# Kernel tuning notes

Measured on AMD Instinct MI355X. Metric: run time of the kernel, lower is better.

Reference implementation:

```python
import jax, jax.numpy as jnp
import numpy as np

D_MODEL = 1024
N_HEADS = 16
D_K = D_MODEL // N_HEADS
B, S = 4, 2048


def setup_inputs() -> dict:
    key = jax.random.key(0)
    ks = jax.random.split(key, 5)
    scale = 1.0 / np.sqrt(D_MODEL)  # ~xavier scale for square matrices
    return {
        "Q": jax.random.normal(ks[0], (B, S, D_MODEL), dtype=jnp.float32),
        "length": jax.random.randint(ks[1], (B,), 1, S, dtype=jnp.int32),
        "Wq": jax.random.normal(ks[2], (D_MODEL, D_MODEL), dtype=jnp.float32) * scale,
        "bq": jnp.zeros((D_MODEL,), dtype=jnp.float32),
        "Wk": jax.random.normal(ks[3], (D_MODEL, D_MODEL), dtype=jnp.float32) * scale,
        "bk": jnp.zeros((D_MODEL,), dtype=jnp.float32),
        "Wv": jax.random.normal(ks[4], (D_MODEL, D_MODEL), dtype=jnp.float32) * scale,
        "bv": jnp.zeros((D_MODEL,), dtype=jnp.float32),
    }


def reference(Q, length, Wq, bq, Wk, bk, Wv, bv):
    b, s, d = Q.shape
    q_a = Q @ Wq + bq                                   # [b, s, d]
    # split heads: [b, h, s, d_k]
    q_s = q_a.reshape(b, s, N_HEADS, D_K).transpose(0, 2, 1, 3)
    k_s = (Q @ Wk + bk).reshape(b, s, N_HEADS, D_K).transpose(0, 2, 1, 3)
    v_s = (Q @ Wv + bv).reshape(b, s, N_HEADS, D_K).transpose(0, 2, 1, 3)

    # unnormalized exp attention with multiplicative key mask (faithful to source)
    scores = jnp.einsum("bhqd,bhkd->bhqk", q_s, k_s) / np.sqrt(D_K)
    scores = jnp.exp(scores)
    key_mask = (jnp.arange(s)[None, :] < length[:, None]).astype(scores.dtype)  # [b, k]
    scores = scores * key_mask[:, None, None, :]        # broadcast over heads, queries
    attn = scores / (jnp.sum(scores, axis=-1, keepdims=True) + 1e-8)
    context = jnp.einsum("bhqk,bhkd->bhqd", attn, v_s)
    context = context.transpose(0, 2, 1, 3).reshape(b, s, d)
    return context, q_a
```

## Files before the change

### kernel.cpp

```cpp
#include <hip/hip_runtime.h>

#define D_MODEL 1024
#define N_HEADS 16
#define D_KH    64
#define BATCH   4
#define SEQ     2048
#define M_TOTAL (BATCH*SEQ)

typedef __attribute__((ext_vector_type(8))) short short8;
typedef __attribute__((ext_vector_type(4))) float f32x4;
typedef __attribute__((ext_vector_type(4))) unsigned short u16x4;

__device__ __forceinline__ unsigned short f2bf(float f) {
  union { float f; unsigned u; } v; v.f = f;
  unsigned r = v.u + 0x7FFFu + ((v.u >> 16) & 1u);
  return (unsigned short)(r >> 16);
}

__global__ __launch_bounds__(256) void cvt_q(const float* __restrict__ Q,
                                             unsigned short* __restrict__ Qbf) {
  size_t i = (size_t)blockIdx.x * 256 + threadIdx.x;
  float4 v = ((const float4*)Q)[i];
  u16x4 o;
  o[0] = f2bf(v.x); o[1] = f2bf(v.y); o[2] = f2bf(v.z); o[3] = f2bf(v.w);
  ((u16x4*)Qbf)[i] = o;
}

__global__ __launch_bounds__(256) void cvt_wt(const float* __restrict__ Wq,
                                              const float* __restrict__ Wk,
                                              const float* __restrict__ Wv,
                                              unsigned short* __restrict__ WT) {
  const int z = blockIdx.z;
  const float* W = (z == 0) ? Wq : (z == 1) ? Wk : Wv;
  __shared__ float tile[32][33];
  const int k0 = blockIdx.y * 32, n0 = blockIdx.x * 32;
  const int tx = threadIdx.x & 31, ty = threadIdx.x >> 5;
  for (int i = 0; i < 4; ++i)
    tile[ty + i * 8][tx] = W[(size_t)(k0 + ty + i * 8) * D_MODEL + n0 + tx];
  __syncthreads();
  unsigned short* out = WT + (size_t)z * D_MODEL * D_MODEL;
  for (int i = 0; i < 4; ++i)
    out[(size_t)(n0 + ty + i * 8) * D_MODEL + k0 + tx] = f2bf(tile[tx][ty + i * 8]);
}

#define BM 128
#define BN 128
#define BK 32

__global__ __launch_bounds__(256, 2) void gemm_qkv(
    const unsigned short* __restrict__ Qbf,
    const unsigned short* __restrict__ WT,
    const float* __restrict__ bq_p, const float* __restrict__ bk_p,
    const float* __restrict__ bv_p,
    float* __restrict__ out_qa,
    unsigned short* __restrict__ kbf,
    unsigned short* __restrict__ vt) {
  const int z  = blockIdx.z;
  const int n0 = blockIdx.x * BN;
  const int m0 = blockIdx.y * BM;
  const int K  = D_MODEL;

  __shared__ unsigned short smA[BM * BK];
  __shared__ unsigned short smB[BN * BK];

  const int t    = threadIdx.x;
  const int lane = t & 63;
  const int w    = t >> 6;
  const int quad = lane >> 4;
  const int l16  = lane & 15;
  const int wr   = w >> 1, wc = w & 1;

  const unsigned short* Wz = WT + (size_t)z * D_MODEL * D_MODEL;

  f32x4 acc[4][4];
  for (int i = 0; i < 4; ++i)
    for (int j = 0; j < 4; ++j) acc[i][j] = (f32x4){0.f, 0.f, 0.f, 0.f};

  for (int k0 = 0; k0 < K; k0 += BK) {
    __syncthreads();
    for (int it = 0; it < 2; ++it) {
      int c   = t + it * 256;
      int row = c >> 2, col = (c & 3) * 8;
      const unsigned short* ga = Qbf + (size_t)(m0 + row) * K + k0 + col;
      const unsigned short* gb = Wz  + (size_t)(n0 + row) * K + k0 + col;
      __builtin_amdgcn_global_load_lds(
          (const __attribute__((address_space(1))) void*)ga,
          (__attribute__((address_space(3))) void*)&smA[c * 8], 16, 0, 0);
      __builtin_amdgcn_global_load_lds(
          (const __attribute__((address_space(1))) void*)gb,
          (__attribute__((address_space(3))) void*)&smB[c * 8], 16, 0, 0);
    }
    __syncthreads();

    short8 afr[4], bfr[4];
    for (int mi = 0; mi < 4; ++mi)
      afr[mi] = *(const short8*)&smA[(wr * 64 + mi * 16 + l16) * BK + quad * 8];
    for (int ni = 0; ni < 4; ++ni)
      bfr[ni] = *(const short8*)&smB[(wc * 64 + ni * 16 + l16) * BK + quad * 8];
    for (int mi = 0; mi < 4; ++mi)
      for (int ni = 0; ni < 4; ++ni)
        acc[mi][ni] = __builtin_amdgcn_mfma_f32_16x16x32_bf16(
            afr[mi], bfr[ni], acc[mi][ni], 0, 0, 0);
  }

  const float* bias = (z == 0) ? bq_p : (z == 1) ? bk_p : bv_p;
  if (z == 2) {
    for (int ni = 0; ni < 4; ++ni) {
      int n = n0 + wc * 64 + ni * 16 + l16;
      float bval = bias[n];
      int h = n >> 6, d = n & 63;
      for (int mi = 0; mi < 4; ++mi) {
        int m = m0 + wr * 64 + mi * 16 + quad * 4;
        int b = m >> 11, s = m & 2047;
        u16x4 o;
        for (int j = 0; j < 4; ++j) o[j] = f2bf(acc[mi][ni][j] + bval);
        *(u16x4*)&vt[(size_t)((b * 16 + h) * 64 + d) * SEQ + s] = o;
      }
    }
  } else {
    for (int ni = 0; ni < 4; ++ni) {
      int n = n0 + wc * 64 + ni * 16 + l16;
      float bval = bias[n];
      for (int mi = 0; mi < 4; ++mi) {
        int mbase = m0 + wr * 64 + mi * 16 + quad * 4;
        for (int j = 0; j < 4; ++j) {
          float v = acc[mi][ni][j] + bval;
          size_t idx = (size_t)(mbase + j) * D_MODEL + n;
          if (z == 0) out_qa[idx] = v;
          else        kbf[idx] = f2bf(v);
        }
      }
    }
  }
}

#define PSTR 72

__global__ __launch_bounds__(256, 2) void attn(
    const float* __restrict__ qa,
    const unsigned short* __restrict__ kbf,
    const unsigned short* __restrict__ vt,
    const int* __restrict__ length,
    float* __restrict__ ctx) {
  const int qt = blockIdx.x;
  const int bh = blockIdx.y;
  const int b = bh >> 4, h = bh & 15;
  const int len = length[b];

  const int t    = threadIdx.x;
  const int lane = t & 63;
  const int w    = t >> 6;
  const int quad = lane >> 4;
  const int l16  = lane & 15;

  __shared__ unsigned short sQ[64 * 64];
  __shared__ unsigned short sK[64 * 64];
  __shared__ unsigned short sVT[64 * 64];
  __shared__ unsigned short sP[64 * PSTR];

  {
    int r = t >> 2, c0 = (t & 3) * 16;
    const float* src = qa + (size_t)(b * SEQ + qt * 64 + r) * D_MODEL + h * D_KH + c0;
    unsigned short* dst = &sQ[r * 64 + c0];
    for (int i = 0; i < 4; ++i) {
      float4 v = *(const float4*)(src + i * 4);
      dst[i * 4 + 0] = f2bf(v.x); dst[i * 4 + 1] = f2bf(v.y);
      dst[i * 4 + 2] = f2bf(v.z); dst[i * 4 + 3] = f2bf(v.w);
    }
  }

  f32x4 accpv[4];
  for (int i = 0; i < 4; ++i) accpv[i] = (f32x4){0.f, 0.f, 0.f, 0.f};
  float den[4] = {0.f, 0.f, 0.f, 0.f};

  const float SCL = 0.125f * 1.44269504f;

  const int nkt = (len + 63) >> 6;
  for (int kt = 0; kt < nkt; ++kt) {
    __syncthreads();
    {
      int r = t >> 2, c0 = (t & 3) * 16;
      size_t koff = (size_t)(b * SEQ + kt * 64 + r) * D_MODEL + h * D_KH + c0;
      *(short8*)&sK[r * 64 + c0]     = *(const short8*)(kbf + koff);
      *(short8*)&sK[r * 64 + c0 + 8] = *(const short8*)(kbf + koff + 8);
      size_t voff = (size_t)(bh * 64 + r) * SEQ + kt * 64 + c0;
      *(short8*)&sVT[r * 64 + c0]     = *(const short8*)(vt + voff);
      *(short8*)&sVT[r * 64 + c0 + 8] = *(const short8*)(vt + voff + 8);
    }
    __syncthreads();

    short8 qa0 = *(const short8*)&sQ[(w * 16 + l16) * 64 + quad * 8];
    short8 qa1 = *(const short8*)&sQ[(w * 16 + l16) * 64 + 32 + quad * 8];
    for (int n = 0; n < 4; ++n) {
      f32x4 s = (f32x4){0.f, 0.f, 0.f, 0.f};
      short8 kb0 = *(const short8*)&sK[(n * 16 + l16) * 64 + quad * 8];
      short8 kb1 = *(const short8*)&sK[(n * 16 + l16) * 64 + 32 + quad * 8];
      s = __builtin_amdgcn_mfma_f32_16x16x32_bf16(qa0, kb0, s, 0, 0, 0);
      s = __builtin_amdgcn_mfma_f32_16x16x32_bf16(qa1, kb1, s, 0, 0, 0);
      int key = kt * 64 + n * 16 + l16;
      bool valid = key < len;
      for (int j = 0; j < 4; ++j) {
        float e = valid ? exp2f(s[j] * SCL) : 0.f;
        den[j] += e;
        sP[(w * 16 + quad * 4 + j) * PSTR + n * 16 + l16] = f2bf(e);
      }
    }

    short8 pa0 = *(const short8*)&sP[(w * 16 + l16) * PSTR + quad * 8];
    short8 pa1 = *(const short8*)&sP[(w * 16 + l16) * PSTR + 32 + quad * 8];
    for (int n2 = 0; n2 < 4; ++n2) {
      short8 vb0 = *(const short8*)&sVT[(n2 * 16 + l16) * 64 + quad * 8];
      short8 vb1 = *(const short8*)&sVT[(n2 * 16 + l16) * 64 + 32 + quad * 8];
      accpv[n2] = __builtin_amdgcn_mfma_f32_16x16x32_bf16(pa0, vb0, accpv[n2], 0, 0, 0);
      accpv[n2] = __builtin_amdgcn_mfma_f32_16x16x32_bf16(pa1, vb1, accpv[n2], 0, 0, 0);
    }
  }

  float inv[4];
  for (int j = 0; j < 4; ++j) {
    float d = den[j];
    d += __shfl_xor(d, 1, 64);
    d += __shfl_xor(d, 2, 64);
    d += __shfl_xor(d, 4, 64);
    d += __shfl_xor(d, 8, 64);
    inv[j] = 1.f / (d + 1e-8f);
  }
  for (int n2 = 0; n2 < 4; ++n2)
    for (int j = 0; j < 4; ++j) {
      int q = qt * 64 + w * 16 + quad * 4 + j;
      int d = h * D_KH + n2 * 16 + l16;
      ctx[(size_t)(b * SEQ + q) * D_MODEL + d] = accpv[n2][j] * inv[j];
    }
}

extern "C" void kernel_launch(void* const* d_in, const int* in_sizes, int n_in,
                              void* d_out, int out_size, void* d_ws, size_t ws_size,
                              hipStream_t stream) {
  const float* Q      = (const float*)d_in[0];
  const int*   length = (const int*)d_in[1];
  const float* Wq     = (const float*)d_in[2];
  const float* bq     = (const float*)d_in[3];
  const float* Wk     = (const float*)d_in[4];
  const float* bk     = (const float*)d_in[5];
  const float* Wv     = (const float*)d_in[6];
  const float* bv     = (const float*)d_in[7];

  float* out_ctx = (float*)d_out;
  float* out_qa  = out_ctx + (size_t)M_TOTAL * D_MODEL;

  char* ws = (char*)d_ws;
  unsigned short* Qbf = (unsigned short*)ws;
  unsigned short* WT  = (unsigned short*)(ws + (size_t)16 * 1024 * 1024);
  unsigned short* Kbf = (unsigned short*)(ws + (size_t)22 * 1024 * 1024);
  unsigned short* Vt  = (unsigned short*)(ws + (size_t)38 * 1024 * 1024);

  hipLaunchKernelGGL(cvt_q, dim3((M_TOTAL * D_MODEL) / (256 * 4)), dim3(256), 0, stream,
                     Q, Qbf);
  hipLaunchKernelGGL(cvt_wt, dim3(32, 32, 3), dim3(256), 0, stream, Wq, Wk, Wv, WT);
  hipLaunchKernelGGL(gemm_qkv, dim3(D_MODEL / BN, M_TOTAL / BM, 3), dim3(256), 0, stream,
                     Qbf, WT, bq, bk, bv, out_qa, Kbf, Vt);
  hipLaunchKernelGGL(attn, dim3(SEQ / 64, BATCH * N_HEADS), dim3(256), 0, stream,
                     out_qa, Kbf, Vt, length, out_ctx);
}
```

Before: 300.2 us.

## Transpose attention MFMAs, pad LDS tiles, pack P stores and vectorize output

```diff
diff --git a/kernel.cpp b/kernel.cpp
--- a/kernel.cpp
+++ b/kernel.cpp
@@ -10,11 +10,15 @@
 typedef __attribute__((ext_vector_type(8))) short short8;
 typedef __attribute__((ext_vector_type(4))) float f32x4;
 typedef __attribute__((ext_vector_type(4))) unsigned short u16x4;
+typedef __attribute__((ext_vector_type(2))) unsigned int u32x2;
 
 __device__ __forceinline__ unsigned short f2bf(float f) {
   union { float f; unsigned u; } v; v.f = f;
   unsigned r = v.u + 0x7FFFu + ((v.u >> 16) & 1u);
   return (unsigned short)(r >> 16);
+}
+__device__ __forceinline__ unsigned fbits(float f) {
+  union { float f; unsigned u; } v; v.f = f; return v.u;
 }
 
 __global__ __launch_bounds__(256) void cvt_q(const float* __restrict__ Q,
@@ -134,7 +138,7 @@
   }
 }
 
-#define PSTR 72
+#define PST 72
 
 __global__ __launch_bounds__(256, 2) void attn(
     const float* __restrict__ qa,
@@ -152,85 +156,90 @@
   const int w    = t >> 6;
   const int quad = lane >> 4;
   const int l16  = lane & 15;
-
-  __shared__ unsigned short sQ[64 * 64];
-  __shared__ unsigned short sK[64 * 64];
-  __shared__ unsigned short sVT[64 * 64];
-  __shared__ unsigned short sP[64 * PSTR];
-
-  {
-    int r = t >> 2, c0 = (t & 3) * 16;
-    const float* src = qa + (size_t)(b * SEQ + qt * 64 + r) * D_MODEL + h * D_KH + c0;
-    unsigned short* dst = &sQ[r * 64 + c0];
-    for (int i = 0; i < 4; ++i) {
-      float4 v = *(const float4*)(src + i * 4);
-      dst[i * 4 + 0] = f2bf(v.x); dst[i * 4 + 1] = f2bf(v.y);
-      dst[i * 4 + 2] = f2bf(v.z); dst[i * 4 + 3] = f2bf(v.w);
-    }
-  }
+  const int r8   = t >> 3;
+  const int c8   = (t & 7) * 8;
+
+  __shared__ unsigned short sQ[64 * PST];
+  __shared__ unsigned short sK[64 * PST];
+  __shared__ unsigned short sVT[64 * PST];
+  __shared__ unsigned short sP[64 * PST];
+
+  for (int half = 0; half < 2; ++half) {
+    int r = r8 + half * 32;
+    const float* src = qa + (size_t)(b * SEQ + qt * 64 + r) * D_MODEL + h * D_KH + c8;
+    float4 v0 = *(const float4*)src;
+    float4 v1 = *(const float4*)(src + 4);
+    short8 o;
+    o[0] = (short)f2bf(v0.x); o[1] = (short)f2bf(v0.y);
+    o[2] = (short)f2bf(v0.z); o[3] = (short)f2bf(v0.w);
+    o[4] = (short)f2bf(v1.x); o[5] = (short)f2bf(v1.y);
+    o[6] = (short)f2bf(v1.z); o[7] = (short)f2bf(v1.w);
+    *(short8*)&sQ[r * PST + c8] = o;
+  }
+  __syncthreads();
+
+  short8 qf0 = *(const short8*)&sQ[(w * 16 + l16) * PST + quad * 8];
+  short8 qf1 = *(const short8*)&sQ[(w * 16 + l16) * PST + 32 + quad * 8];
 
   f32x4 accpv[4];
   for (int i = 0; i < 4; ++i) accpv[i] = (f32x4){0.f, 0.f, 0.f, 0.f};
-  float den[4] = {0.f, 0.f, 0.f, 0.f};
+  float den = 0.f;
 
   const float SCL = 0.125f * 1.44269504f;
 
   const int nkt = (len + 63) >> 6;
   for (int kt = 0; kt < nkt; ++kt) {
     __syncthreads();
-    {
-      int r = t >> 2, c0 = (t & 3) * 16;
-      size_t koff = (size_t)(b * SEQ + kt * 64 + r) * D_MODEL + h * D_KH + c0;
-      *(short8*)&sK[r * 64 + c0]     = *(const short8*)(kbf + koff);
-      *(short8*)&sK[r * 64 + c0 + 8] = *(const short8*)(kbf + koff + 8);
-      size_t voff = (size_t)(bh * 64 + r) * SEQ + kt * 64 + c0;
-      *(short8*)&sVT[r * 64 + c0]     = *(const short8*)(vt + voff);
-      *(short8*)&sVT[r * 64 + c0 + 8] = *(const short8*)(vt + voff + 8);
-    }
-    __syncthreads();
-
-    short8 qa0 = *(const short8*)&sQ[(w * 16 + l16) * 64 + quad * 8];
-    short8 qa1 = *(const short8*)&sQ[(w * 16 + l16) * 64 + 32 + quad * 8];
+    for (int half = 0; half < 2; ++half) {
+      int r = r8 + half * 32;
+      size_t koff = (size_t)(b * SEQ + kt * 64 + r) * D_MODEL + h * D_KH + c8;
+      *(short8*)&sK[r * PST + c8] = *(const short8*)(kbf + koff);
+      size_t voff = (size_t)(bh * 64 + r) * SEQ + kt * 64 + c8;
+      *(short8*)&sVT[r * PST + c8] = *(const short8*)(vt + voff);
+    }
+    __syncthreads();
+
     for (int n = 0; n < 4; ++n) {
+      short8 kf0 = *(const short8*)&sK[(n * 16 + l16) * PST + quad * 8];
+      short8 kf1 = *(const short8*)&sK[(n * 16 + l16) * PST + 32 + quad * 8];
       f32x4 s = (f32x4){0.f, 0.f, 0.f, 0.f};
-      short8 kb0 = *(const short8*)&sK[(n * 16 + l16) * 64 + quad * 8];
-      short8 kb1 = *(const short8*)&sK[(n * 16 + l16) * 64 + 32 + quad * 8];
-      s = __builtin_amdgcn_mfma_f32_16x16x32_bf16(qa0, kb0, s, 0, 0, 0);
-      s = __builtin_amdgcn_mfma_f32_16x16x32_bf16(qa1, kb1, s, 0, 0, 0);
-      int key = kt * 64 + n * 16 + l16;
-      bool valid = key < len;
-      for (int j = 0; j < 4; ++j) {
-        float e = valid ? exp2f(s[j] * SCL) : 0.f;
-        den[j] += e;
-        sP[(w * 16 + quad * 4 + j) * PSTR + n * 16 + l16] = f2bf(e);
-      }
-    }
-
-    short8 pa0 = *(const short8*)&sP[(w * 16 + l16) * PSTR + quad * 8];
-    short8 pa1 = *(const short8*)&sP[(w * 16 + l16) * PSTR + 32 + quad * 8];
+      s = __builtin_amdgcn_mfma_f32_16x16x32_bf16(kf0, qf0, s, 0, 0, 0);
+      s = __builtin_amdgcn_mfma_f32_16x16x32_bf16(kf1, qf1, s, 0, 0, 0);
+      int kbase = kt * 64 + n * 16 + quad * 4;
+      float e0 = (kbase + 0 < len) ? exp2f(s[0] * SCL) : 0.f;
+      float e1 = (kbase + 1 < len) ? exp2f(s[1] * SCL) : 0.f;
+      float e2 = (kbase + 2 < len) ? exp2f(s[2] * SCL) : 0.f;
+      float e3 = (kbase + 3 < len) ? exp2f(s[3] * SCL) : 0.f;
+      den += (e0 + e1) + (e2 + e3);
+      u32x2 pk;
+      pk[0] = __builtin_amdgcn_perm(fbits(e1), fbits(e0), 0x07060302);
+      pk[1] = __builtin_amdgcn_perm(fbits(e3), fbits(e2), 0x07060302);
+      *(u32x2*)&sP[(w * 16 + l16) * PST + n * 16 + quad * 4] = pk;
+    }
+
+    short8 pf0 = *(const short8*)&sP[(w * 16 + l16) * PST + quad * 8];
+    short8 pf1 = *(const short8*)&sP[(w * 16 + l16) * PST + 32 + quad * 8];
     for (int n2 = 0; n2 < 4; ++n2) {
-      short8 vb0 = *(const short8*)&sVT[(n2 * 16 + l16) * 64 + quad * 8];
-      short8 vb1 = *(const short8*)&sVT[(n2 * 16 + l16) * 64 + 32 + quad * 8];
-      accpv[n2] = __builtin_amdgcn_mfma_f32_16x16x32_bf16(pa0, vb0, accpv[n2], 0, 0, 0);
-      accpv[n2] = __builtin_amdgcn_mfma_f32_16x16x32_bf16(pa1, vb1, accpv[n2], 0, 0, 0);
-    }
-  }
-
-  float inv[4];
-  for (int j = 0; j < 4; ++j) {
-    float d = den[j];
-    d += __shfl_xor(d, 1, 64);
-    d += __shfl_xor(d, 2, 64);
-    d += __shfl_xor(d, 4, 64);
-    d += __shfl_xor(d, 8, 64);
-    inv[j] = 1.f / (d + 1e-8f);
-  }
-  for (int n2 = 0; n2 < 4; ++n2)
-    for (int j = 0; j < 4; ++j) {
-      int q = qt * 64 + w * 16 + quad * 4 + j;
-      int d = h * D_KH + n2 * 16 + l16;
-      ctx[(size_t)(b * SEQ + q) * D_MODEL + d] = accpv[n2][j] * inv[j];
-    }
+      short8 vf0 = *(const short8*)&sVT[(n2 * 16 + l16) * PST + quad * 8];
+      short8 vf1 = *(const short8*)&sVT[(n2 * 16 + l16) * PST + 32 + quad * 8];
+      accpv[n2] = __builtin_amdgcn_mfma_f32_16x16x32_bf16(vf0, pf0, accpv[n2], 0, 0, 0);
+      accpv[n2] = __builtin_amdgcn_mfma_f32_16x16x32_bf16(vf1, pf1, accpv[n2], 0, 0, 0);
+    }
+  }
+
+  den += __shfl_xor(den, 16, 64);
+  den += __shfl_xor(den, 32, 64);
+  float inv = 1.f / (den + 1e-8f);
+
+  {
+    int q = qt * 64 + w * 16 + l16;
+    float* dst = ctx + (size_t)(b * SEQ + q) * D_MODEL + h * D_KH;
+    for (int n2 = 0; n2 < 4; ++n2) {
+      f32x4 o = accpv[n2];
+      float4 v = make_float4(o[0] * inv, o[1] * inv, o[2] * inv, o[3] * inv);
+      *(float4*)(dst + n2 * 16 + quad * 4) = v;
+    }
+  }
 }
 
 extern "C" void kernel_launch(void* const* d_in, const int* in_sizes, int n_in,
```

Measured after the change: 261.1 us. 13.0% less time.
